# Optimization experiments

Measured on AMD Instinct MI355X. Metric: run time of the kernel, lower is better.

The kernel has to match this reference:

```python
import jax, jax.numpy as jnp
import numpy as np

N_EMBED = 1024
HEAD_SIZE = 64
BLOCK_SIZE = 2048


def setup_inputs() -> dict:
    key = jax.random.key(0)
    kx, kk, kv = jax.random.split(key, 3)
    x = jax.random.normal(kx, (8, 2048, N_EMBED), dtype=jnp.float32)
    # nn.Linear(n_embed, head_size, bias=False): weight [head_size, n_embed]
    scale = 1.0 / np.sqrt(N_EMBED)
    W_k = jax.random.uniform(kk, (HEAD_SIZE, N_EMBED), dtype=jnp.float32, minval=-scale, maxval=scale)
    W_v = jax.random.uniform(kv, (HEAD_SIZE, N_EMBED), dtype=jnp.float32, minval=-scale, maxval=scale)
    return {"x": x, "W_k": W_k, "W_v": W_v}


def reference(x, W_k, W_v):
    # Faithful to source: q = self.key(x) (query projection is unused in the original forward)
    T = x.shape[1]
    k = jnp.einsum('btc,hc->bth', x, W_k)   # [B,T,H]
    q = k                                    # source bug: q uses key projection
    wei = jnp.einsum('bth,bsh->bts', q, k) * (HEAD_SIZE ** -0.5)  # [B,T,T]
    causal = jnp.tril(jnp.ones((T, T), dtype=bool))
    wei = jnp.where(causal, wei, -jnp.inf)
    wei = jax.nn.softmax(wei, axis=-1)
    v = jnp.einsum('btc,hc->bth', x, W_v)
    out = jnp.einsum('bts,bsh->bth', wei, v)
    return out
```

## Files before the change

kernel.cpp:

```cpp
#include <hip/hip_runtime.h>


typedef __bf16 bf16;
typedef __bf16 bf16x4 __attribute__((ext_vector_type(4)));
typedef __bf16 bf16x8 __attribute__((ext_vector_type(8)));
typedef float  floatx4 __attribute__((ext_vector_type(4)));

#define T_LEN 2048
#define HEAD  64
#define CEMB  1024

static __device__ __forceinline__ bf16x8 cvt2(float4 a, float4 b) {
    bf16x8 r;
    r[0] = (bf16)a.x; r[1] = (bf16)a.y; r[2] = (bf16)a.z; r[3] = (bf16)a.w;
    r[4] = (bf16)b.x; r[5] = (bf16)b.y; r[6] = (bf16)b.z; r[7] = (bf16)b.w;
    return r;
}

__global__ __launch_bounds__(256) void wconv_kernel(const float* __restrict__ Wk,
                                                    const float* __restrict__ Wv,
                                                    bf16* __restrict__ Wb) {
    int i = (blockIdx.x * 256 + threadIdx.x) * 4;
    const float* src = (i < 64 * 1024) ? (Wk + i) : (Wv + (i - 64 * 1024));
    float4 f = *(const float4*)src;
    bf16x4 v;
    v[0] = (bf16)f.x; v[1] = (bf16)f.y; v[2] = (bf16)f.z; v[3] = (bf16)f.w;
    *(bf16x4*)&Wb[i] = v;
}

__global__ __launch_bounds__(256) void proj_kernel(const float* __restrict__ x,
                                                   const bf16* __restrict__ Wb,
                                                   bf16* __restrict__ Kbuf,
                                                   bf16* __restrict__ Vt) {
    __shared__ __align__(16) bf16 As[2][32][72];
    __shared__ __align__(16) bf16 Bs[2][128][72];

    const int tid  = threadIdx.x;
    const int wave = tid >> 6;
    const int lane = tid & 63;
    const int quad = lane >> 4;
    const int low  = lane & 15;

    const long row0 = (long)blockIdx.x * 32;

    const int a_row = tid >> 3;
    const int a_col = (tid & 7) * 8;
    const int b_row = tid >> 1;
    const int b_col = (tid & 1) * 32;

    const float* abase = x + (row0 + a_row) * CEMB + a_col;
    const bf16*  bbase = Wb + b_row * CEMB + b_col;

    const int strip = wave & 1;
    const int nq    = (wave >> 1) * 4;

    floatx4 acc[4];
#pragma unroll
    for (int i = 0; i < 4; ++i) acc[i] = (floatx4){0.f, 0.f, 0.f, 0.f};

    float4 apf0 = ((const float4*)abase)[0], apf1 = ((const float4*)abase)[1];
    float4 bpf0 = ((const float4*)bbase)[0], bpf1 = ((const float4*)bbase)[1];
    float4 bpf2 = ((const float4*)bbase)[2], bpf3 = ((const float4*)bbase)[3];
    *(bf16x8*)&As[0][a_row][a_col] = cvt2(apf0, apf1);
    *(float4*)&Bs[0][b_row][b_col]      = bpf0;
    *(float4*)&Bs[0][b_row][b_col + 8]  = bpf1;
    *(float4*)&Bs[0][b_row][b_col + 16] = bpf2;
    *(float4*)&Bs[0][b_row][b_col + 24] = bpf3;
    __syncthreads();

    int buf = 0;
    for (int s = 0; s < 16; ++s) {
        const bool more = (s < 15);
        if (more) {
            const int k0 = (s + 1) * 64;
            apf0 = ((const float4*)(abase + k0))[0]; apf1 = ((const float4*)(abase + k0))[1];
            bpf0 = ((const float4*)(bbase + k0))[0]; bpf1 = ((const float4*)(bbase + k0))[1];
            bpf2 = ((const float4*)(bbase + k0))[2]; bpf3 = ((const float4*)(bbase + k0))[3];
        }
#pragma unroll
        for (int ks = 0; ks < 2; ++ks) {
            bf16x8 afrag = *(const bf16x8*)&As[buf][strip * 16 + low][ks * 32 + quad * 8];
#pragma unroll
            for (int i = 0; i < 4; ++i) {
                bf16x8 bfrag = *(const bf16x8*)&Bs[buf][(nq + i) * 16 + low][ks * 32 + quad * 8];
                acc[i] = __builtin_amdgcn_mfma_f32_16x16x32_bf16(afrag, bfrag, acc[i], 0, 0, 0);
            }
        }
        if (more) {
            const int nb = buf ^ 1;
            *(bf16x8*)&As[nb][a_row][a_col] = cvt2(apf0, apf1);
            *(float4*)&Bs[nb][b_row][b_col]      = bpf0;
            *(float4*)&Bs[nb][b_row][b_col + 8]  = bpf1;
            *(float4*)&Bs[nb][b_row][b_col + 16] = bpf2;
            *(float4*)&Bs[nb][b_row][b_col + 24] = bpf3;
            __syncthreads();
            buf = nb;
        }
    }

    const long bidx  = row0 >> 11;
    const int  tloc0 = (int)(row0 & 2047);
#pragma unroll
    for (int i = 0; i < 4; ++i) {
#pragma unroll
        for (int r = 0; r < 4; ++r) {
            int trow = tloc0 + strip * 16 + quad * 4 + r;
            int cl   = (nq + i) * 16 + low;
            bf16 val = (bf16)acc[i][r];
            if (cl < HEAD) Kbuf[(bidx * T_LEN + trow) * HEAD + cl] = val;
            else           Vt[(bidx * HEAD + (cl - HEAD)) * T_LEN + trow] = val;
        }
    }
}

__global__ __launch_bounds__(256) void attn_kernel(const bf16* __restrict__ Kbuf,
                                                   const bf16* __restrict__ Vt,
                                                   float* __restrict__ Opart,
                                                   float* __restrict__ lpart) {
    __shared__ __align__(16) bf16 Ks[2][64][72];
    __shared__ __align__(16) bf16 Vs[2][64][72];
    __shared__ __align__(16) bf16 Ps[64][72];

    const int tid  = threadIdx.x;
    const int wave = tid >> 6;
    const int lane = tid & 63;
    const int quad = lane >> 4;
    const int low  = lane & 15;

    const int c  = blockIdx.x & 7;
    const int qb = (blockIdx.x >> 3) & 31;
    const int b  = blockIdx.x >> 8;

    const bf16* kbase = Kbuf + (long)b * T_LEN * HEAD;
    const bf16* vbase = Vt + (long)b * HEAD * T_LEN;

    const bf16* qrow = kbase + (qb * 64 + wave * 16 + low) * HEAD + quad * 8;
    const bf16x8 qf0 = *(const bf16x8*)(qrow);
    const bf16x8 qf1 = *(const bf16x8*)(qrow + 32);

    bf16x8 ones;
#pragma unroll
    for (int i = 0; i < 8; ++i) ones[i] = (bf16)1.0f;

    floatx4 o[4], ol;
#pragma unroll
    for (int nt = 0; nt < 4; ++nt) o[nt] = (floatx4){0.f, 0.f, 0.f, 0.f};
    ol = (floatx4){0.f, 0.f, 0.f, 0.f};

    const int s_row = tid >> 2;
    const int s_col = (tid & 3) * 16;
    const bf16* ksrc = kbase + s_row * HEAD + s_col;
    const bf16* vsrc = vbase + (long)s_row * T_LEN + s_col;

    if (c <= qb) {
        float4 kpf0 = *(const float4*)(ksrc + c * 4096);
        float4 kpf1 = *(const float4*)(ksrc + c * 4096 + 8);
        float4 vpf0 = *(const float4*)(vsrc + c * 64);
        float4 vpf1 = *(const float4*)(vsrc + c * 64 + 8);
        *(float4*)&Ks[0][s_row][s_col]     = kpf0;
        *(float4*)&Ks[0][s_row][s_col + 8] = kpf1;
        *(float4*)&Vs[0][s_row][s_col]     = vpf0;
        *(float4*)&Vs[0][s_row][s_col + 8] = vpf1;
        __syncthreads();

        int buf = 0;
        for (int j = c; j <= qb; j += 8) {
            const bool more = (j + 8 <= qb);
            if (more) {
                kpf0 = *(const float4*)(ksrc + (j + 8) * 4096);
                kpf1 = *(const float4*)(ksrc + (j + 8) * 4096 + 8);
                vpf0 = *(const float4*)(vsrc + (j + 8) * 64);
                vpf1 = *(const float4*)(vsrc + (j + 8) * 64 + 8);
            }

            floatx4 s_[4];
#pragma unroll
            for (int nt = 0; nt < 4; ++nt) {
                bf16x8 kf0 = *(const bf16x8*)&Ks[buf][nt * 16 + low][quad * 8];
                bf16x8 kf1 = *(const bf16x8*)&Ks[buf][nt * 16 + low][32 + quad * 8];
                floatx4 z = (floatx4){0.f, 0.f, 0.f, 0.f};
                z = __builtin_amdgcn_mfma_f32_16x16x32_bf16(qf0, kf0, z, 0, 0, 0);
                z = __builtin_amdgcn_mfma_f32_16x16x32_bf16(qf1, kf1, z, 0, 0, 0);
                s_[nt] = z;
            }

            const bool diag = (j == qb);
#pragma unroll
            for (int nt = 0; nt < 4; ++nt) {
#pragma unroll
                for (int r = 0; r < 4; ++r) {
                    float p = __builtin_amdgcn_exp2f(s_[nt][r] * 0.180336880f);
                    if (diag && (nt * 16 + low) > (wave * 16 + quad * 4 + r)) p = 0.f;
                    Ps[wave * 16 + quad * 4 + r][nt * 16 + low] = (bf16)p;
                }
            }

            bf16x8 pf0 = *(const bf16x8*)&Ps[wave * 16 + low][quad * 8];
            bf16x8 pf1 = *(const bf16x8*)&Ps[wave * 16 + low][32 + quad * 8];
#pragma unroll
            for (int nt = 0; nt < 4; ++nt) {
                bf16x8 vf0 = *(const bf16x8*)&Vs[buf][nt * 16 + low][quad * 8];
                bf16x8 vf1 = *(const bf16x8*)&Vs[buf][nt * 16 + low][32 + quad * 8];
                o[nt] = __builtin_amdgcn_mfma_f32_16x16x32_bf16(pf0, vf0, o[nt], 0, 0, 0);
                o[nt] = __builtin_amdgcn_mfma_f32_16x16x32_bf16(pf1, vf1, o[nt], 0, 0, 0);
            }
            ol = __builtin_amdgcn_mfma_f32_16x16x32_bf16(pf0, ones, ol, 0, 0, 0);
            ol = __builtin_amdgcn_mfma_f32_16x16x32_bf16(pf1, ones, ol, 0, 0, 0);

            if (more) {
                const int nb = buf ^ 1;
                *(float4*)&Ks[nb][s_row][s_col]     = kpf0;
                *(float4*)&Ks[nb][s_row][s_col + 8] = kpf1;
                *(float4*)&Vs[nb][s_row][s_col]     = vpf0;
                *(float4*)&Vs[nb][s_row][s_col + 8] = vpf1;
                __syncthreads();
                buf = nb;
            }
        }
    }

    float* ob = Opart + (long)blockIdx.x * 4096;
#pragma unroll
    for (int nt = 0; nt < 4; ++nt) {
#pragma unroll
        for (int r = 0; r < 4; ++r) {
            int row = wave * 16 + quad * 4 + r;
            ob[row * 64 + nt * 16 + low] = o[nt][r];
        }
    }
    if (low == 0) {
#pragma unroll
        for (int r = 0; r < 4; ++r)
            lpart[(long)blockIdx.x * 64 + wave * 16 + quad * 4 + r] = ol[r];
    }
}

__global__ __launch_bounds__(256) void attn_combine(const float* __restrict__ Opart,
                                                    const float* __restrict__ lpart,
                                                    float* __restrict__ out) {
    const int tile = blockIdx.x;
    const int tid  = threadIdx.x;
    const int row  = tid >> 2;
    const int col0 = (tid & 3) * 16;

    const float* ob = Opart + (long)tile * 8 * 4096 + row * 64 + col0;
    const float* lb = lpart + (long)tile * 8 * 64 + row;

    float l = 0.f;
#pragma unroll
    for (int ch = 0; ch < 8; ++ch) l += lb[ch * 64];
    float rl = 1.0f / l;

    float4 s0 = (float4){0.f, 0.f, 0.f, 0.f}, s1 = s0, s2 = s0, s3 = s0;
#pragma unroll
    for (int ch = 0; ch < 8; ++ch) {
        const float4* p = (const float4*)(ob + ch * 4096);
        float4 a = p[0], b = p[1], c = p[2], d = p[3];
        s0.x += a.x; s0.y += a.y; s0.z += a.z; s0.w += a.w;
        s1.x += b.x; s1.y += b.y; s1.z += b.z; s1.w += b.w;
        s2.x += c.x; s2.y += c.y; s2.z += c.z; s2.w += c.w;
        s3.x += d.x; s3.y += d.y; s3.z += d.z; s3.w += d.w;
    }
    s0.x *= rl; s0.y *= rl; s0.z *= rl; s0.w *= rl;
    s1.x *= rl; s1.y *= rl; s1.z *= rl; s1.w *= rl;
    s2.x *= rl; s2.y *= rl; s2.z *= rl; s2.w *= rl;
    s3.x *= rl; s3.y *= rl; s3.z *= rl; s3.w *= rl;

    float4* op = (float4*)(out + (long)tile * 4096 + row * 64 + col0);
    op[0] = s0; op[1] = s1; op[2] = s2; op[3] = s3;
}

extern "C" void kernel_launch(void* const* d_in, const int* in_sizes, int n_in,
                              void* d_out, int out_size, void* d_ws, size_t ws_size,
                              hipStream_t stream) {
    const float* x  = (const float*)d_in[0];
    const float* Wk = (const float*)d_in[1];
    const float* Wv = (const float*)d_in[2];
    float* out = (float*)d_out;

    char* ws = (char*)d_ws;
    bf16*  Wb    = (bf16*)ws;
    bf16*  Kbuf  = (bf16*)(ws + (1 << 20));
    bf16*  Vt    = (bf16*)(ws + (3 << 20));
    float* Opart = (float*)(ws + (5 << 20));
    float* lpart = (float*)(ws + (37 << 20));

    wconv_kernel<<<128, 256, 0, stream>>>(Wk, Wv, Wb);
    proj_kernel<<<512, 256, 0, stream>>>(x, Wb, Kbuf, Vt);
    attn_kernel<<<2048, 256, 0, stream>>>(Kbuf, Vt, Opart, lpart);
    attn_combine<<<256, 256, 0, stream>>>(Opart, lpart, out);
}
```

Before: 145.2 us.

## Drop LDS staging; load MFMA fragments directly from global memory

```diff
diff --git a/kernel.cpp b/kernel.cpp
--- a/kernel.cpp
+++ b/kernel.cpp
@@ -28,88 +28,66 @@
     *(bf16x4*)&Wb[i] = v;
 }
 
-__global__ __launch_bounds__(256) void proj_kernel(const float* __restrict__ x,
-                                                   const bf16* __restrict__ Wb,
-                                                   bf16* __restrict__ Kbuf,
-                                                   bf16* __restrict__ Vt) {
-    __shared__ __align__(16) bf16 As[2][32][72];
-    __shared__ __align__(16) bf16 Bs[2][128][72];
-
+__global__ __launch_bounds__(256, 4) void proj_kernel(const float* __restrict__ x,
+                                                      const bf16* __restrict__ Wb,
+                                                      bf16* __restrict__ Kbuf,
+                                                      bf16* __restrict__ Vt) {
     const int tid  = threadIdx.x;
     const int wave = tid >> 6;
     const int lane = tid & 63;
     const int quad = lane >> 4;
     const int low  = lane & 15;
 
-    const long row0 = (long)blockIdx.x * 32;
-
-    const int a_row = tid >> 3;
-    const int a_col = (tid & 7) * 8;
-    const int b_row = tid >> 1;
-    const int b_col = (tid & 1) * 32;
-
-    const float* abase = x + (row0 + a_row) * CEMB + a_col;
-    const bf16*  bbase = Wb + b_row * CEMB + b_col;
-
-    const int strip = wave & 1;
-    const int nq    = (wave >> 1) * 4;
+    const int mhalf = wave >> 1;
+    const int nhalf = wave & 1;
+    const long row0 = (long)blockIdx.x * 32 + mhalf * 16;
+
+    const float* arow = x + (row0 + low) * CEMB + quad * 8;
+    const bf16*  wrow = Wb + ((nhalf * 64) + low) * CEMB + quad * 8;
 
     floatx4 acc[4];
 #pragma unroll
     for (int i = 0; i < 4; ++i) acc[i] = (floatx4){0.f, 0.f, 0.f, 0.f};
 
-    float4 apf0 = ((const float4*)abase)[0], apf1 = ((const float4*)abase)[1];
-    float4 bpf0 = ((const float4*)bbase)[0], bpf1 = ((const float4*)bbase)[1];
-    float4 bpf2 = ((const float4*)bbase)[2], bpf3 = ((const float4*)bbase)[3];
-    *(bf16x8*)&As[0][a_row][a_col] = cvt2(apf0, apf1);
-    *(float4*)&Bs[0][b_row][b_col]      = bpf0;
-    *(float4*)&Bs[0][b_row][b_col + 8]  = bpf1;
-    *(float4*)&Bs[0][b_row][b_col + 16] = bpf2;
-    *(float4*)&Bs[0][b_row][b_col + 24] = bpf3;
-    __syncthreads();
-
-    int buf = 0;
-    for (int s = 0; s < 16; ++s) {
-        const bool more = (s < 15);
-        if (more) {
-            const int k0 = (s + 1) * 64;
-            apf0 = ((const float4*)(abase + k0))[0]; apf1 = ((const float4*)(abase + k0))[1];
-            bpf0 = ((const float4*)(bbase + k0))[0]; bpf1 = ((const float4*)(bbase + k0))[1];
-            bpf2 = ((const float4*)(bbase + k0))[2]; bpf3 = ((const float4*)(bbase + k0))[3];
-        }
-#pragma unroll
-        for (int ks = 0; ks < 2; ++ks) {
-            bf16x8 afrag = *(const bf16x8*)&As[buf][strip * 16 + low][ks * 32 + quad * 8];
-#pragma unroll
-            for (int i = 0; i < 4; ++i) {
-                bf16x8 bfrag = *(const bf16x8*)&Bs[buf][(nq + i) * 16 + low][ks * 32 + quad * 8];
-                acc[i] = __builtin_amdgcn_mfma_f32_16x16x32_bf16(afrag, bfrag, acc[i], 0, 0, 0);
-            }
-        }
-        if (more) {
-            const int nb = buf ^ 1;
-            *(bf16x8*)&As[nb][a_row][a_col] = cvt2(apf0, apf1);
-            *(float4*)&Bs[nb][b_row][b_col]      = bpf0;
-            *(float4*)&Bs[nb][b_row][b_col + 8]  = bpf1;
-            *(float4*)&Bs[nb][b_row][b_col + 16] = bpf2;
-            *(float4*)&Bs[nb][b_row][b_col + 24] = bpf3;
-            __syncthreads();
-            buf = nb;
-        }
-    }
-
-    const long bidx  = row0 >> 11;
-    const int  tloc0 = (int)(row0 & 2047);
-#pragma unroll
-    for (int i = 0; i < 4; ++i) {
-#pragma unroll
-        for (int r = 0; r < 4; ++r) {
-            int trow = tloc0 + strip * 16 + quad * 4 + r;
-            int cl   = (nq + i) * 16 + low;
-            bf16 val = (bf16)acc[i][r];
-            if (cl < HEAD) Kbuf[(bidx * T_LEN + trow) * HEAD + cl] = val;
-            else           Vt[(bidx * HEAD + (cl - HEAD)) * T_LEN + trow] = val;
-        }
+    float4 a0[2], a1[2];
+    bf16x8 bfr[2][4];
+
+    a0[0] = *(const float4*)(arow);
+    a1[0] = *(const float4*)(arow + 4);
+#pragma unroll
+    for (int nt = 0; nt < 4; ++nt) bfr[0][nt] = *(const bf16x8*)(wrow + nt * 16 * CEMB);
+
+#pragma unroll 2
+    for (int c = 0; c < 32; ++c) {
+        const int cur = c & 1, nxt = cur ^ 1;
+        if (c < 31) {
+            const int k0 = (c + 1) * 32;
+            a0[nxt] = *(const float4*)(arow + k0);
+            a1[nxt] = *(const float4*)(arow + k0 + 4);
+#pragma unroll
+            for (int nt = 0; nt < 4; ++nt)
+                bfr[nxt][nt] = *(const bf16x8*)(wrow + nt * 16 * CEMB + k0);
+        }
+        bf16x8 af = cvt2(a0[cur], a1[cur]);
+#pragma unroll
+        for (int nt = 0; nt < 4; ++nt)
+            acc[nt] = __builtin_amdgcn_mfma_f32_16x16x32_bf16(af, bfr[cur][nt], acc[nt], 0, 0, 0);
+    }
+
+    const long bidx = row0 >> 11;
+    const int  tl0  = (int)(row0 & 2047) + quad * 4;
+    if (nhalf == 0) {
+#pragma unroll
+        for (int nt = 0; nt < 4; ++nt)
+#pragma unroll
+            for (int r = 0; r < 4; ++r)
+                Kbuf[(bidx * T_LEN + tl0 + r) * HEAD + nt * 16 + low] = (bf16)acc[nt][r];
+    } else {
+#pragma unroll
+        for (int nt = 0; nt < 4; ++nt)
+#pragma unroll
+            for (int r = 0; r < 4; ++r)
+                Vt[(bidx * HEAD + nt * 16 + low) * T_LEN + tl0 + r] = (bf16)acc[nt][r];
     }
 }
 
@@ -117,9 +95,7 @@
                                                    const bf16* __restrict__ Vt,
                                                    float* __restrict__ Opart,
                                                    float* __restrict__ lpart) {
-    __shared__ __align__(16) bf16 Ks[2][64][72];
-    __shared__ __align__(16) bf16 Vs[2][64][72];
-    __shared__ __align__(16) bf16 Ps[64][72];
+    __shared__ __align__(16) bf16 Ps[4][16][72];
 
     const int tid  = threadIdx.x;
     const int wave = tid >> 6;
@@ -147,76 +123,43 @@
     for (int nt = 0; nt < 4; ++nt) o[nt] = (floatx4){0.f, 0.f, 0.f, 0.f};
     ol = (floatx4){0.f, 0.f, 0.f, 0.f};
 
-    const int s_row = tid >> 2;
-    const int s_col = (tid & 3) * 16;
-    const bf16* ksrc = kbase + s_row * HEAD + s_col;
-    const bf16* vsrc = vbase + (long)s_row * T_LEN + s_col;
-
-    if (c <= qb) {
-        float4 kpf0 = *(const float4*)(ksrc + c * 4096);
-        float4 kpf1 = *(const float4*)(ksrc + c * 4096 + 8);
-        float4 vpf0 = *(const float4*)(vsrc + c * 64);
-        float4 vpf1 = *(const float4*)(vsrc + c * 64 + 8);
-        *(float4*)&Ks[0][s_row][s_col]     = kpf0;
-        *(float4*)&Ks[0][s_row][s_col + 8] = kpf1;
-        *(float4*)&Vs[0][s_row][s_col]     = vpf0;
-        *(float4*)&Vs[0][s_row][s_col + 8] = vpf1;
-        __syncthreads();
-
-        int buf = 0;
-        for (int j = c; j <= qb; j += 8) {
-            const bool more = (j + 8 <= qb);
-            if (more) {
-                kpf0 = *(const float4*)(ksrc + (j + 8) * 4096);
-                kpf1 = *(const float4*)(ksrc + (j + 8) * 4096 + 8);
-                vpf0 = *(const float4*)(vsrc + (j + 8) * 64);
-                vpf1 = *(const float4*)(vsrc + (j + 8) * 64 + 8);
+    for (int j = c; j <= qb; j += 8) {
+        const bf16* kr = kbase + (j * 64 + low) * HEAD + quad * 8;
+        floatx4 s_[4];
+#pragma unroll
+        for (int nt = 0; nt < 4; ++nt) {
+            bf16x8 kf0 = *(const bf16x8*)(kr + nt * 16 * HEAD);
+            bf16x8 kf1 = *(const bf16x8*)(kr + nt * 16 * HEAD + 32);
+            floatx4 z = (floatx4){0.f, 0.f, 0.f, 0.f};
+            z = __builtin_amdgcn_mfma_f32_16x16x32_bf16(qf0, kf0, z, 0, 0, 0);
+            z = __builtin_amdgcn_mfma_f32_16x16x32_bf16(qf1, kf1, z, 0, 0, 0);
+            s_[nt] = z;
+        }
+
+        const bool diag = (j == qb);
+#pragma unroll
+        for (int nt = 0; nt < 4; ++nt) {
+#pragma unroll
+            for (int r = 0; r < 4; ++r) {
+                float p = __builtin_amdgcn_exp2f(s_[nt][r] * 0.180336880f);
+                if (diag && (nt * 16 + low) > (wave * 16 + quad * 4 + r)) p = 0.f;
+                Ps[wave][quad * 4 + r][nt * 16 + low] = (bf16)p;
             }
-
-            floatx4 s_[4];
-#pragma unroll
-            for (int nt = 0; nt < 4; ++nt) {
-                bf16x8 kf0 = *(const bf16x8*)&Ks[buf][nt * 16 + low][quad * 8];
-                bf16x8 kf1 = *(const bf16x8*)&Ks[buf][nt * 16 + low][32 + quad * 8];
-                floatx4 z = (floatx4){0.f, 0.f, 0.f, 0.f};
-                z = __builtin_amdgcn_mfma_f32_16x16x32_bf16(qf0, kf0, z, 0, 0, 0);
-                z = __builtin_amdgcn_mfma_f32_16x16x32_bf16(qf1, kf1, z, 0, 0, 0);
-                s_[nt] = z;
-            }
-
-            const bool diag = (j == qb);
-#pragma unroll
-            for (int nt = 0; nt < 4; ++nt) {
-#pragma unroll
-                for (int r = 0; r < 4; ++r) {
-                    float p = __builtin_amdgcn_exp2f(s_[nt][r] * 0.180336880f);
-                    if (diag && (nt * 16 + low) > (wave * 16 + quad * 4 + r)) p = 0.f;
-                    Ps[wave * 16 + quad * 4 + r][nt * 16 + low] = (bf16)p;
-                }
-            }
-
-            bf16x8 pf0 = *(const bf16x8*)&Ps[wave * 16 + low][quad * 8];
-            bf16x8 pf1 = *(const bf16x8*)&Ps[wave * 16 + low][32 + quad * 8];
-#pragma unroll
-            for (int nt = 0; nt < 4; ++nt) {
-                bf16x8 vf0 = *(const bf16x8*)&Vs[buf][nt * 16 + low][quad * 8];
-                bf16x8 vf1 = *(const bf16x8*)&Vs[buf][nt * 16 + low][32 + quad * 8];
-                o[nt] = __builtin_amdgcn_mfma_f32_16x16x32_bf16(pf0, vf0, o[nt], 0, 0, 0);
-                o[nt] = __builtin_amdgcn_mfma_f32_16x16x32_bf16(pf1, vf1, o[nt], 0, 0, 0);
-            }
-            ol = __builtin_amdgcn_mfma_f32_16x16x32_bf16(pf0, ones, ol, 0, 0, 0);
-            ol = __builtin_amdgcn_mfma_f32_16x16x32_bf16(pf1, ones, ol, 0, 0, 0);
-
-            if (more) {
-                const int nb = buf ^ 1;
-                *(float4*)&Ks[nb][s_row][s_col]     = kpf0;
-                *(float4*)&Ks[nb][s_row][s_col + 8] = kpf1;
-                *(float4*)&Vs[nb][s_row][s_col]     = vpf0;
-                *(float4*)&Vs[nb][s_row][s_col + 8] = vpf1;
-                __syncthreads();
-                buf = nb;
-            }
-        }
+        }
+
+        bf16x8 pf0 = *(const bf16x8*)&Ps[wave][low][quad * 8];
+        bf16x8 pf1 = *(const bf16x8*)&Ps[wave][low][32 + quad * 8];
+
+        const bf16* vr = vbase + (long)low * T_LEN + j * 64 + quad * 8;
+#pragma unroll
+        for (int nt = 0; nt < 4; ++nt) {
+            bf16x8 vf0 = *(const bf16x8*)(vr + (long)nt * 16 * T_LEN);
+            bf16x8 vf1 = *(const bf16x8*)(vr + (long)nt * 16 * T_LEN + 32);
+            o[nt] = __builtin_amdgcn_mfma_f32_16x16x32_bf16(pf0, vf0, o[nt], 0, 0, 0);
+            o[nt] = __builtin_amdgcn_mfma_f32_16x16x32_bf16(pf1, vf1, o[nt], 0, 0, 0);
+        }
+        ol = __builtin_amdgcn_mfma_f32_16x16x32_bf16(pf0, ones, ol, 0, 0, 0);
+        ol = __builtin_amdgcn_mfma_f32_16x16x32_bf16(pf1, ones, ol, 0, 0, 0);
     }
 
     float* ob = Opart + (long)blockIdx.x * 4096;
```

Result: slower. 191.1 us (+31.6%).
